# Kernel tuning notes

Hardware: AMD Instinct MI355X
Metric: run time of the kernel (lower is better)

The kernel has to match this reference:

```python
import jax, jax.numpy as jnp
import numpy as np

B, D, L = 4, 512, 4096
N1, N2 = 1167, 8921


def setup_inputs() -> dict:
    key = jax.random.key(0)
    k1, k2, k3, k4 = jax.random.split(key, 4)
    H = jax.random.normal(k1, (B, D, L), dtype=jnp.float32)
    Q1_w = jax.random.normal(k2, (N1, D), dtype=jnp.float32) * (1.0 / np.sqrt(D))
    Q2_w = jax.random.normal(k3, (N2, D), dtype=jnp.float32) * (1.0 / np.sqrt(D))
    Q12_w = jax.random.normal(k4, (N2, N1), dtype=jnp.float32) * (1.0 / np.sqrt(N1))
    return {"H": H, "Q1_w": Q1_w, "Q2_w": Q2_w, "Q12_w": Q12_w}


def reference(H, Q1_w, Q2_w, Q12_w):
    # H: [b, d, l]; Q1_w: [n1, d]; Q2_w: [n2, d]; Q12_w: [n2, n1]
    # Level-1 label attention
    E1 = jnp.einsum('nd,bdl->bnl', Q1_w, H)          # [b, n1, l]
    A1 = jax.nn.softmax(E1, axis=2)
    C1 = jnp.einsum('bnl,bdl->bnd', A1, H)           # [b, n1, d]
    # Project level-1 context to level-2 label space
    C1 = jnp.einsum('mn,bnd->bmd', Q12_w, C1)        # [b, n2, d]
    # Level-2 queries modulated by level-1 context (elementwise)
    Q2 = Q2_w[None, :, :] * C1                       # [b, n2, d]
    E2 = jnp.einsum('bmd,bdl->bml', Q2, H)           # [b, n2, l]
    A2 = jax.nn.softmax(E2, axis=2)
    C2 = jnp.einsum('bml,bdl->bmd', A2, H)           # [b, n2, d]
    return (C2, A2)
```

## Files before the change

kernel.cpp:

```cpp
#include <hip/hip_runtime.h>
#include <hip/hip_bf16.h>

typedef __bf16 bf16_t;
typedef __bf16 bf16x8 __attribute__((ext_vector_type(8)));
typedef __bf16 bf16x4 __attribute__((ext_vector_type(4)));
typedef float  f32x4  __attribute__((ext_vector_type(4)));

#define BM 128
#define BN 128
#define BK 64

__global__ __launch_bounds__(256) void cast_transpose_H(
    const float* __restrict__ H, bf16_t* __restrict__ Hb,
    bf16_t* __restrict__ HTb, int D, int L) {
  __shared__ bf16_t tile[32][33];
  int b = blockIdx.z;
  int l0 = blockIdx.x * 32, d0 = blockIdx.y * 32;
  const float* Hp = H + (size_t)b * D * L;
  bf16_t* Hbp = Hb + (size_t)b * D * L;
  bf16_t* HTp = HTb + (size_t)b * L * D;
  int tx = threadIdx.x, ty = threadIdx.y;
#pragma unroll
  for (int r = 0; r < 4; r++) {
    int d = d0 + ty + r * 8;
    float v = Hp[(size_t)d * L + l0 + tx];
    bf16_t bv = (bf16_t)v;
    tile[ty + r * 8][tx] = bv;
    Hbp[(size_t)d * L + l0 + tx] = bv;
  }
  __syncthreads();
#pragma unroll
  for (int r = 0; r < 4; r++) {
    int l = l0 + ty + r * 8;
    HTp[(size_t)l * D + d0 + tx] = tile[tx][ty + r * 8];
  }
}

__global__ void cast_w(const float* __restrict__ in, bf16_t* __restrict__ out, int n) {
  int i = blockIdx.x * 256 + threadIdx.x;
  if (i < n) out[i] = (bf16_t)in[i];
}

__global__ void cast_w_pad(const float* __restrict__ in, bf16_t* __restrict__ out,
                           int cols, int ldo) {
  int c = blockIdx.x * 256 + threadIdx.x;
  int r = blockIdx.y;
  if (c < ldo) {
    float v = (c < cols) ? in[(size_t)r * cols + c] : 0.0f;
    out[(size_t)r * ldo + c] = (bf16_t)v;
  }
}

__global__ void zero_pad(bf16_t* __restrict__ p, int n1, int ld, int rows) {
  int i = blockIdx.x * 256 + threadIdx.x;
  int padw = ld - n1;
  int r = i / padw, c = i - r * padw;
  if (r < rows) p[(size_t)r * ld + n1 + c] = (bf16_t)0.0f;
}

__device__ inline bf16x8 cvt8(float4 a, float4 b) {
  bf16x8 o;
  o[0] = (bf16_t)a.x; o[1] = (bf16_t)a.y; o[2] = (bf16_t)a.z; o[3] = (bf16_t)a.w;
  o[4] = (bf16_t)b.x; o[5] = (bf16_t)b.y; o[6] = (bf16_t)b.z; o[7] = (bf16_t)b.w;
  return o;
}

__device__ inline void gload_lds16(const bf16_t* g, bf16_t* l) {
  __builtin_amdgcn_global_load_lds(
      (const __attribute__((address_space(1))) void*)g,
      (__attribute__((address_space(3))) void*)l, 16, 0, 0);
}

__device__ inline void stage_half(const bf16_t* __restrict__ src, int ld,
                                  bf16_t* lds_half, int t, int wid) {
  int r = t >> 3;
  int gsl = (t & 7) ^ (r & 7);
  const bf16_t* g = src + (size_t)r * ld + gsl * 8;
  gload_lds16(g, lds_half + wid * 512);
  gload_lds16(g + (size_t)64 * ld, lds_half + 4096 + wid * 512);
}

template <int EPI>
__global__ __launch_bounds__(512) void gemm256_bt(
    const bf16_t* __restrict__ A, long sAb, const bf16_t* __restrict__ BT, long sBb,
    void* __restrict__ Cv, long sCb, const float* __restrict__ W,
    int M, int N, int K, int lda, int ldb, int ldc) {
  __shared__ __align__(16) bf16_t As[2][256][64];
  __shared__ __align__(16) bf16_t Bs[2][256][64];
  int b = blockIdx.z;
  A += (size_t)b * sAb;
  BT += (size_t)b * sBb;

  int nx = gridDim.x, ny = gridDim.y;
  int nwg = nx * ny;
  int bid = blockIdx.x + nx * blockIdx.y;
  int qq = nwg >> 3, rr = nwg & 7;
  int xcd = bid & 7, lin = bid >> 3;
  int swz = (xcd < rr ? xcd * (qq + 1) : rr * (qq + 1) + (xcd - rr) * qq) + lin;
  int m0 = (swz / ny) * 256;
  int n0 = (swz % ny) * 256;

  int t = threadIdx.x;
  int lane = t & 63, wid = t >> 6;
  int l15 = lane & 15, q = lane >> 4;
  int wm = (wid >> 2) * 128;
  int wn = (wid & 3) * 64;
  int NT = K >> 6;

  f32x4 acc[8][4];
#pragma unroll
  for (int i = 0; i < 8; i++)
#pragma unroll
    for (int j = 0; j < 4; j++)
#pragma unroll
      for (int e = 0; e < 4; e++) acc[i][j][e] = 0.0f;

  stage_half(BT + (size_t)(n0 + 0) * ldb, ldb, &Bs[0][0][0], t, wid);
  stage_half(BT + (size_t)(n0 + 128) * ldb, ldb, &Bs[0][128][0], t, wid);
  stage_half(A + (size_t)(m0 + 0) * lda, lda, &As[0][0][0], t, wid);
  stage_half(A + (size_t)(m0 + 128) * lda, lda, &As[0][128][0], t, wid);
  stage_half(BT + (size_t)(n0 + 0) * ldb + 64, ldb, &Bs[1][0][0], t, wid);
  stage_half(BT + (size_t)(n0 + 128) * ldb + 64, ldb, &Bs[1][128][0], t, wid);
  asm volatile("s_waitcnt vmcnt(4)" ::: "memory");
  __builtin_amdgcn_s_barrier();

  bf16x8 af[4][2];
  bf16x8 bF[2][2][2];

  for (int kt = 0; kt < NT; ++kt) {
    int buf = kt & 1;
    const bf16_t* An = A + (size_t)m0 * lda + (size_t)(kt + 1) * 64;
    const bf16_t* Bn2 = BT + (size_t)n0 * ldb + (size_t)(kt + 2) * 64;

    auto readA = [&](int mh) {
#pragma unroll
      for (int i = 0; i < 4; i++) {
        const char* rowp = (const char*)&As[buf][wm + mh * 64 + i * 16 + l15][0];
#pragma unroll
        for (int ks = 0; ks < 2; ks++)
          af[i][ks] = *(const bf16x8*)(rowp + ((((ks * 4 + q) ^ (l15 & 7))) << 4));
      }
    };
    auto readB = [&](int ch) {
#pragma unroll
      for (int j = 0; j < 2; j++) {
        const char* rowp = (const char*)&Bs[buf][wn + ch * 32 + j * 16 + l15][0];
#pragma unroll
        for (int ks = 0; ks < 2; ks++)
          bF[ch][j][ks] = *(const bf16x8*)(rowp + ((((ks * 4 + q) ^ (l15 & 7))) << 4));
      }
    };
    auto mmaq = [&](int mh, int ch) {
      __builtin_amdgcn_s_setprio(1);
#pragma unroll
      for (int i = 0; i < 4; i++)
#pragma unroll
        for (int j = 0; j < 2; j++)
#pragma unroll
          for (int ks = 0; ks < 2; ks++)
            acc[mh * 4 + i][ch * 2 + j] = __builtin_amdgcn_mfma_f32_16x16x32_bf16(
                af[i][ks], bF[ch][j][ks], acc[mh * 4 + i][ch * 2 + j], 0, 0, 0);
      __builtin_amdgcn_s_setprio(0);
    };

    readA(0);
    readB(0);
    if (kt + 1 < NT) stage_half(An, lda, &As[buf ^ 1][0][0], t, wid);
    __builtin_amdgcn_s_barrier();
    mmaq(0, 0);
    __builtin_amdgcn_s_barrier();
    readB(1);
    if (kt + 1 < NT) stage_half(An + (size_t)128 * lda, lda, &As[buf ^ 1][128][0], t, wid);
    __builtin_amdgcn_s_barrier();
    mmaq(0, 1);
    __builtin_amdgcn_s_barrier();
    readA(1);
    if (kt + 2 < NT) stage_half(Bn2, ldb, &Bs[buf][0][0], t, wid);
    __builtin_amdgcn_s_barrier();
    mmaq(1, 0);
    __builtin_amdgcn_s_barrier();
    if (kt + 2 < NT) {
      stage_half(Bn2 + (size_t)128 * ldb, ldb, &Bs[buf][128][0], t, wid);
      asm volatile("s_waitcnt vmcnt(4)" ::: "memory");
    } else if (kt + 1 < NT) {
      asm volatile("s_waitcnt vmcnt(0)" ::: "memory");
    }
    __builtin_amdgcn_s_barrier();
    mmaq(1, 1);
    __builtin_amdgcn_s_barrier();
  }

#pragma unroll
  for (int ig = 0; ig < 8; ig++) {
    int rbase = m0 + wm + ig * 16 + q * 4;
#pragma unroll
    for (int jg = 0; jg < 4; jg++) {
      int c = n0 + wn + jg * 16 + l15;
#pragma unroll
      for (int r4 = 0; r4 < 4; r4++) {
        int r = rbase + r4;
        if (r < M) {
          float val = acc[ig][jg][r4];
          if (EPI == 0) {
            ((float*)Cv + (size_t)b * sCb)[(size_t)r * ldc + c] = val;
          } else {
            float w = W[(size_t)r * N + c];
            ((bf16_t*)Cv + (size_t)b * sCb)[(size_t)r * ldc + c] = (bf16_t)(val * w);
          }
        }
      }
    }
  }
}

template <typename AT, int EPI>
__global__ __launch_bounds__(256) void gemm_bt(
    const AT* __restrict__ A, long sAb, const bf16_t* __restrict__ BT, long sBb,
    void* __restrict__ Cv, long sCb, const float* __restrict__ W,
    int M, int N, int K, int lda, int ldb, int ldc) {
  constexpr bool AF32 = (sizeof(AT) == 4);
  __shared__ __align__(16) bf16_t As[BM][BK];
  __shared__ __align__(16) bf16_t Bs[BN][BK];
  int b = blockIdx.z;
  A += (size_t)b * sAb;
  BT += (size_t)b * sBb;

  int nx = gridDim.x, ny = gridDim.y;
  int nwg = nx * ny;
  int bid = blockIdx.x + nx * blockIdx.y;
  int qq = nwg >> 3, rr = nwg & 7;
  int xcd = bid & 7, lin = bid >> 3;
  int swz = (xcd < rr ? xcd * (qq + 1) : rr * (qq + 1) + (xcd - rr) * qq) + lin;
  int m0 = (swz / ny) * BM;
  int n0 = (swz % ny) * BN;

  int t = threadIdx.x;
  int lane = t & 63, wid = t >> 6;
  int l15 = lane & 15, q = lane >> 4;
  int wm = (wid >> 1) * 64, wn = (wid & 1) * 64;

  int r0 = t >> 3;
  int sl = t & 7;
  int gsl = sl ^ (r0 & 7);
  bf16_t* lA = &As[0][0] + (size_t)wid * 512;
  bf16_t* lB = &Bs[0][0] + (size_t)wid * 512;

  f32x4 acc[4][4];
#pragma unroll
  for (int i = 0; i < 4; i++)
#pragma unroll
    for (int j = 0; j < 4; j++)
#pragma unroll
      for (int e = 0; e < 4; e++) acc[i][j][e] = 0.0f;

  for (int kb = 0; kb < K; kb += BK) {
    float4 va[4][2];
    if constexpr (AF32) {
#pragma unroll
      for (int i = 0; i < 4; i++) {
        int gm = m0 + i * 32 + r0;
        if (gm < M) {
          const float4* p = (const float4*)(A + (size_t)gm * lda + kb + gsl * 8);
          va[i][0] = p[0];
          va[i][1] = p[1];
        } else {
          va[i][0] = make_float4(0.f, 0.f, 0.f, 0.f);
          va[i][1] = make_float4(0.f, 0.f, 0.f, 0.f);
        }
      }
    }
    __syncthreads();
#pragma unroll
    for (int i = 0; i < 4; i++)
      gload_lds16(BT + (size_t)(n0 + i * 32 + r0) * ldb + kb + gsl * 8,
                  lB + i * 2048);
    if constexpr (AF32) {
#pragma unroll
      for (int i = 0; i < 4; i++)
        *(bf16x8*)(&As[0][0] + (size_t)(i * 256 + t) * 8) = cvt8(va[i][0], va[i][1]);
    } else {
#pragma unroll
      for (int i = 0; i < 4; i++)
        gload_lds16(A + (size_t)(m0 + i * 32 + r0) * lda + kb + gsl * 8,
                    lA + i * 2048);
    }
    __syncthreads();

#pragma unroll
    for (int ks = 0; ks < 2; ks++) {
      bf16x8 af[4], bfr[4];
#pragma unroll
      for (int i = 0; i < 4; i++) {
        int row = wm + i * 16 + l15;
        int off = (ks * 64 + q * 16) ^ ((l15 & 7) << 4);
        af[i] = *(const bf16x8*)((const char*)&As[row][0] + off);
      }
#pragma unroll
      for (int j = 0; j < 4; j++) {
        int row = wn + j * 16 + l15;
        int off = (ks * 64 + q * 16) ^ ((l15 & 7) << 4);
        bfr[j] = *(const bf16x8*)((const char*)&Bs[row][0] + off);
      }
#pragma unroll
      for (int i = 0; i < 4; i++)
#pragma unroll
        for (int j = 0; j < 4; j++)
          acc[i][j] = __builtin_amdgcn_mfma_f32_16x16x32_bf16(af[i], bfr[j],
                                                              acc[i][j], 0, 0, 0);
    }
  }

#pragma unroll
  for (int i = 0; i < 4; i++) {
    int rbase = m0 + wm + i * 16 + q * 4;
#pragma unroll
    for (int j = 0; j < 4; j++) {
      int c = n0 + wn + j * 16 + l15;
#pragma unroll
      for (int r4 = 0; r4 < 4; r4++) {
        int r = rbase + r4;
        if (r < M) {
          float val = acc[i][j][r4];
          if (EPI == 0) {
            float* Cp = (float*)Cv + (size_t)b * sCb;
            Cp[(size_t)r * ldc + c] = val;
          } else if (EPI == 1) {
            bf16_t* Cp = (bf16_t*)Cv + (size_t)b * sCb;
            Cp[(size_t)c * ldc + r] = (bf16_t)val;
          } else {
            float w = W[(size_t)r * N + c];
            bf16_t* Cp = (bf16_t*)Cv + (size_t)b * sCb;
            Cp[(size_t)r * ldc + c] = (bf16_t)(val * w);
          }
        }
      }
    }
  }
}

template <int MODE>
__global__ __launch_bounds__(256) void softmax_rows(
    const float* __restrict__ in, void* __restrict__ out,
    bf16_t* __restrict__ out2, int L) {
  int row = blockIdx.x;
  const float* ip = in + (size_t)row * L;
  int t = threadIdx.x;
  int lane = t & 63, wid = t >> 6;
  float4 v[4];
  float m = -3.4e38f;
#pragma unroll
  for (int c = 0; c < 4; c++) {
    v[c] = ((const float4*)ip)[c * 256 + t];
    m = fmaxf(m, fmaxf(fmaxf(v[c].x, v[c].y), fmaxf(v[c].z, v[c].w)));
  }
#pragma unroll
  for (int off = 1; off < 64; off <<= 1) m = fmaxf(m, __shfl_xor(m, off));
  __shared__ float redm[4];
  __shared__ float reds[4];
  if (lane == 0) redm[wid] = m;
  __syncthreads();
  m = fmaxf(fmaxf(redm[0], redm[1]), fmaxf(redm[2], redm[3]));
  float s = 0.0f;
#pragma unroll
  for (int c = 0; c < 4; c++) {
    v[c].x = __expf(v[c].x - m);
    v[c].y = __expf(v[c].y - m);
    v[c].z = __expf(v[c].z - m);
    v[c].w = __expf(v[c].w - m);
    s += (v[c].x + v[c].y) + (v[c].z + v[c].w);
  }
#pragma unroll
  for (int off = 1; off < 64; off <<= 1) s += __shfl_xor(s, off);
  if (lane == 0) reds[wid] = s;
  __syncthreads();
  s = (reds[0] + reds[1]) + (reds[2] + reds[3]);
  float inv = 1.0f / s;
  if (MODE == 1) {
    bf16_t* op = (bf16_t*)out + (size_t)row * L;
#pragma unroll
    for (int c = 0; c < 4; c++) {
      bf16x4 o;
      o[0] = (bf16_t)(v[c].x * inv);
      o[1] = (bf16_t)(v[c].y * inv);
      o[2] = (bf16_t)(v[c].z * inv);
      o[3] = (bf16_t)(v[c].w * inv);
      *(bf16x4*)(op + ((size_t)c * 256 + t) * 4) = o;
    }
  } else {
    float* op = (float*)out + (size_t)row * L;
#pragma unroll
    for (int c = 0; c < 4; c++) {
      float fx = v[c].x * inv, fy = v[c].y * inv, fz = v[c].z * inv, fw = v[c].w * inv;
      ((float4*)op)[c * 256 + t] = make_float4(fx, fy, fz, fw);
      if (MODE == 2) {
        bf16x4 o;
        o[0] = (bf16_t)fx; o[1] = (bf16_t)fy; o[2] = (bf16_t)fz; o[3] = (bf16_t)fw;
        *(bf16x4*)(out2 + (size_t)row * L + ((size_t)c * 256 + t) * 4) = o;
      }
    }
  }
}

extern "C" void kernel_launch(void* const* d_in, const int* in_sizes, int n_in,
                              void* d_out, int out_size, void* d_ws, size_t ws_size,
                              hipStream_t stream) {
  const int B = 4, D = 512, L = 4096, N1 = 1167, N2 = 8921;
  const int N1K = 1216;
  const int M1P = 1280;
  const int M2P = 8960;
  const float* H = (const float*)d_in[0];
  const float* Q1w = (const float*)d_in[1];
  const float* Q2w = (const float*)d_in[2];
  const float* Q12w = (const float*)d_in[3];
  float* C2 = (float*)d_out;
  float* A2 = C2 + (size_t)B * N2 * D;

  char* ws = (char*)d_ws;
  size_t off = 0;
  auto alloc = [&](size_t bytes) -> void* {
    void* p = ws + off;
    off = (off + bytes + 255) & ~(size_t)255;
    return p;
  };
  bf16_t* Hb   = (bf16_t*)alloc((size_t)B * D * L * 2);
  bf16_t* HTb  = (bf16_t*)alloc((size_t)B * L * D * 2);
  bf16_t* Q1b  = (bf16_t*)alloc((size_t)M1P * D * 2);
  bf16_t* Q12b = (bf16_t*)alloc((size_t)M2P * N1K * 2);
  float*  E1   = (float*)alloc((size_t)B * N1 * L * 4);
  bf16_t* A1b  = (bf16_t*)alloc(((size_t)B * N1 + 128) * L * 2);
  bf16_t* C1Tb = (bf16_t*)alloc((size_t)B * D * N1K * 2);
  bf16_t* Q2b  = (bf16_t*)alloc(((size_t)B * N2 + 64) * D * 2);
  size_t a2b_bytes = ((size_t)B * N2 + 128) * (size_t)L * 2;
  bool useA2b = (ws_size > 0) && (off + a2b_bytes <= ws_size);
  bf16_t* A2b = (bf16_t*)alloc(a2b_bytes);

  cast_transpose_H<<<dim3(L / 32, D / 32, B), dim3(32, 8), 0, stream>>>(H, Hb, HTb, D, L);
  cast_w<<<(N1 * D + 255) / 256, 256, 0, stream>>>(Q1w, Q1b, N1 * D);
  cast_w_pad<<<dim3((N1K + 255) / 256, N2), 256, 0, stream>>>(Q12w, Q12b, N1, N1K);
  zero_pad<<<(B * D * (N1K - N1) + 255) / 256, 256, 0, stream>>>(C1Tb, N1, N1K, B * D);
  gemm256_bt<0><<<dim3(M1P / 256, L / 256, B), 512, 0, stream>>>(
      Q1b, 0, HTb, (long)L * D, E1, (long)N1 * L, nullptr, N1, L, D, D, D, L);
  softmax_rows<1><<<B * N1, 256, 0, stream>>>(E1, A1b, nullptr, L);
  gemm_bt<bf16_t, 1><<<dim3(M1P / BM, D / BN, B), 256, 0, stream>>>(
      A1b, (long)N1 * L, Hb, (long)D * L, C1Tb, (long)D * N1K, nullptr, N1, D, L, L, L, N1K);
  gemm256_bt<2><<<dim3(M2P / 256, D / 256, B), 512, 0, stream>>>(
      Q12b, 0, C1Tb, (long)D * N1K, Q2b, (long)N2 * D, Q2w, N2, D, N1K, N1K, N1K, D);
  gemm256_bt<0><<<dim3(M2P / 256, L / 256, B), 512, 0, stream>>>(
      Q2b, (long)N2 * D, HTb, (long)L * D, A2, (long)N2 * L, nullptr, N2, L, D, D, D, L);
  if (useA2b) {
    softmax_rows<2><<<B * N2, 256, 0, stream>>>(A2, A2, A2b, L);
    gemm256_bt<0><<<dim3(M2P / 256, D / 256, B), 512, 0, stream>>>(
        A2b, (long)N2 * L, Hb, (long)D * L, C2, (long)N2 * D, nullptr, N2, D, L, L, L, D);
  } else {
    softmax_rows<0><<<B * N2, 256, 0, stream>>>(A2, A2, nullptr, L);
    gemm_bt<float, 0><<<dim3(M2P / BM, D / BN, B), 256, 0, stream>>>(
        A2, (long)N2 * L, Hb, (long)D * L, C2, (long)N2 * D, nullptr, N2, D, L, L, L, D);
  }
}
```

Measured before the change: 1.713 ms.

## Rework level-1 pipeline layout and move several GEMMs to 128-tile kernel

Pads N1 to 1280 across Q1, Q12 and A1 buffers and zero-fills the padded rows. The softmax writes into the padded per-batch layout, and the A1·H GEMM is recomputed as H·A1ᵀ so C1ᵀ is stored with coalesced row-major writes instead of the transposed scatter. The level-1 E1 GEMM, the Q12 projection and the final A2·H GEMM switch from the 256-tile 512-thread kernel to the 128-tile kernel, which raises block count for the smaller-N launches. The 256-tile kernel's barriers move to inline asm. The tradeoff is extra padded compute and less per-block reuse in the large final GEMM.

```diff
diff --git a/kernel.cpp b/kernel.cpp
--- a/kernel.cpp
+++ b/kernel.cpp
@@ -9,6 +9,8 @@
 #define BM 128
 #define BN 128
 #define BK 64
+
+#define SBAR() asm volatile("s_barrier" ::: "memory")
 
 __global__ __launch_bounds__(256) void cast_transpose_H(
     const float* __restrict__ H, bf16_t* __restrict__ Hb,
@@ -51,11 +53,14 @@
   }
 }
 
-__global__ void zero_pad(bf16_t* __restrict__ p, int n1, int ld, int rows) {
-  int i = blockIdx.x * 256 + threadIdx.x;
-  int padw = ld - n1;
-  int r = i / padw, c = i - r * padw;
-  if (r < rows) p[(size_t)r * ld + n1 + c] = (bf16_t)0.0f;
+__global__ void zero_rows(bf16_t* __restrict__ p, int r0, int nr, long sb, int L) {
+  long i = (long)blockIdx.x * 256 + threadIdx.x;
+  int b = blockIdx.y;
+  long tot = (long)nr * L / 8;
+  if (i < tot) {
+    bf16x8 z = {};
+    *(bf16x8*)(p + ((long)b * sb + r0) * L + i * 8) = z;
+  }
 }
 
 __device__ inline bf16x8 cvt8(float4 a, float4 b) {
@@ -122,7 +127,7 @@
   stage_half(BT + (size_t)(n0 + 0) * ldb + 64, ldb, &Bs[1][0][0], t, wid);
   stage_half(BT + (size_t)(n0 + 128) * ldb + 64, ldb, &Bs[1][128][0], t, wid);
   asm volatile("s_waitcnt vmcnt(4)" ::: "memory");
-  __builtin_amdgcn_s_barrier();
+  SBAR();
 
   bf16x8 af[4][2];
   bf16x8 bF[2][2][2];
@@ -166,28 +171,28 @@
     readA(0);
     readB(0);
     if (kt + 1 < NT) stage_half(An, lda, &As[buf ^ 1][0][0], t, wid);
-    __builtin_amdgcn_s_barrier();
+    SBAR();
     mmaq(0, 0);
-    __builtin_amdgcn_s_barrier();
+    SBAR();
     readB(1);
     if (kt + 1 < NT) stage_half(An + (size_t)128 * lda, lda, &As[buf ^ 1][128][0], t, wid);
-    __builtin_amdgcn_s_barrier();
+    SBAR();
     mmaq(0, 1);
-    __builtin_amdgcn_s_barrier();
+    SBAR();
     readA(1);
     if (kt + 2 < NT) stage_half(Bn2, ldb, &Bs[buf][0][0], t, wid);
-    __builtin_amdgcn_s_barrier();
+    SBAR();
     mmaq(1, 0);
-    __builtin_amdgcn_s_barrier();
+    SBAR();
     if (kt + 2 < NT) {
       stage_half(Bn2 + (size_t)128 * ldb, ldb, &Bs[buf][128][0], t, wid);
       asm volatile("s_waitcnt vmcnt(4)" ::: "memory");
     } else if (kt + 1 < NT) {
       asm volatile("s_waitcnt vmcnt(0)" ::: "memory");
     }
-    __builtin_amdgcn_s_barrier();
+    SBAR();
     mmaq(1, 1);
-    __builtin_amdgcn_s_barrier();
+    SBAR();
   }
 
 #pragma unroll
@@ -201,12 +206,7 @@
         int r = rbase + r4;
         if (r < M) {
           float val = acc[ig][jg][r4];
-          if (EPI == 0) {
-            ((float*)Cv + (size_t)b * sCb)[(size_t)r * ldc + c] = val;
-          } else {
-            float w = W[(size_t)r * N + c];
-            ((bf16_t*)Cv + (size_t)b * sCb)[(size_t)r * ldc + c] = (bf16_t)(val * w);
-          }
+          ((float*)Cv + (size_t)b * sCb)[(size_t)r * ldc + c] = val;
         }
       }
     }
@@ -324,13 +324,13 @@
           if (EPI == 0) {
             float* Cp = (float*)Cv + (size_t)b * sCb;
             Cp[(size_t)r * ldc + c] = val;
-          } else if (EPI == 1) {
-            bf16_t* Cp = (bf16_t*)Cv + (size_t)b * sCb;
-            Cp[(size_t)c * ldc + r] = (bf16_t)val;
-          } else {
+          } else if (EPI == 2) {
             float w = W[(size_t)r * N + c];
             bf16_t* Cp = (bf16_t*)Cv + (size_t)b * sCb;
             Cp[(size_t)r * ldc + c] = (bf16_t)(val * w);
+          } else {
+            bf16_t* Cp = (bf16_t*)Cv + (size_t)b * sCb;
+            Cp[(size_t)r * ldc + c] = (bf16_t)val;
           }
         }
       }
@@ -341,9 +341,10 @@
 template <int MODE>
 __global__ __launch_bounds__(256) void softmax_rows(
     const float* __restrict__ in, void* __restrict__ out,
-    bf16_t* __restrict__ out2, int L) {
-  int row = blockIdx.x;
-  const float* ip = in + (size_t)row * L;
+    bf16_t* __restrict__ out2, int L, int ostr) {
+  long row_in = (long)blockIdx.y * gridDim.x + blockIdx.x;
+  long row_out = (long)blockIdx.y * ostr + blockIdx.x;
+  const float* ip = in + row_in * L;
   int t = threadIdx.x;
   int lane = t & 63, wid = t >> 6;
   float4 v[4];
@@ -376,7 +377,7 @@
   s = (reds[0] + reds[1]) + (reds[2] + reds[3]);
   float inv = 1.0f / s;
   if (MODE == 1) {
-    bf16_t* op = (bf16_t*)out + (size_t)row * L;
+    bf16_t* op = (bf16_t*)out + row_out * L;
 #pragma unroll
     for (int c = 0; c < 4; c++) {
       bf16x4 o;
@@ -387,7 +388,7 @@
       *(bf16x4*)(op + ((size_t)c * 256 + t) * 4) = o;
     }
   } else {
-    float* op = (float*)out + (size_t)row * L;
+    float* op = (float*)out + row_out * L;
 #pragma unroll
     for (int c = 0; c < 4; c++) {
       float fx = v[c].x * inv, fy = v[c].y * inv, fz = v[c].z * inv, fw = v[c].w * inv;
@@ -395,7 +396,7 @@
       if (MODE == 2) {
         bf16x4 o;
         o[0] = (bf16_t)fx; o[1] = (bf16_t)fy; o[2] = (bf16_t)fz; o[3] = (bf16_t)fw;
-        *(bf16x4*)(out2 + (size_t)row * L + ((size_t)c * 256 + t) * 4) = o;
+        *(bf16x4*)(out2 + row_out * L + ((size_t)c * 256 + t) * 4) = o;
       }
     }
   }
@@ -405,8 +406,7 @@
                               void* d_out, int out_size, void* d_ws, size_t ws_size,
                               hipStream_t stream) {
   const int B = 4, D = 512, L = 4096, N1 = 1167, N2 = 8921;
-  const int N1K = 1216;
-  const int M1P = 1280;
+  const int N1P = 1280;
   const int M2P = 8960;
   const float* H = (const float*)d_in[0];
   const float* Q1w = (const float*)d_in[1];
@@ -424,35 +424,39 @@
   };
   bf16_t* Hb   = (bf16_t*)alloc((size_t)B * D * L * 2);
   bf16_t* HTb  = (bf16_t*)alloc((size_t)B * L * D * 2);
-  bf16_t* Q1b  = (bf16_t*)alloc((size_t)M1P * D * 2);
-  bf16_t* Q12b = (bf16_t*)alloc((size_t)M2P * N1K * 2);
+  bf16_t* Q1b  = (bf16_t*)alloc((size_t)N1P * D * 2);
+  bf16_t* Q12b = (bf16_t*)alloc((size_t)M2P * N1P * 2);
   float*  E1   = (float*)alloc((size_t)B * N1 * L * 4);
-  bf16_t* A1b  = (bf16_t*)alloc(((size_t)B * N1 + 128) * L * 2);
-  bf16_t* C1Tb = (bf16_t*)alloc((size_t)B * D * N1K * 2);
+  bf16_t* A1b  = (bf16_t*)alloc((size_t)B * N1P * L * 2);
+  bf16_t* C1Tb = (bf16_t*)alloc((size_t)B * D * N1P * 2);
   bf16_t* Q2b  = (bf16_t*)alloc(((size_t)B * N2 + 64) * D * 2);
   size_t a2b_bytes = ((size_t)B * N2 + 128) * (size_t)L * 2;
   bool useA2b = (ws_size > 0) && (off + a2b_bytes <= ws_size);
   bf16_t* A2b = (bf16_t*)alloc(a2b_bytes);
 
   cast_transpose_H<<<dim3(L / 32, D / 32, B), dim3(32, 8), 0, stream>>>(H, Hb, HTb, D, L);
-  cast_w<<<(N1 * D + 255) / 256, 256, 0, stream>>>(Q1w, Q1b, N1 * D);
-  cast_w_pad<<<dim3((N1K + 255) / 256, N2), 256, 0, stream>>>(Q12w, Q12b, N1, N1K);
-  zero_pad<<<(B * D * (N1K - N1) + 255) / 256, 256, 0, stream>>>(C1Tb, N1, N1K, B * D);
-  gemm256_bt<0><<<dim3(M1P / 256, L / 256, B), 512, 0, stream>>>(
+  cast_w_pad<<<dim3((D + 255) / 256, N1P), 256, 0, stream>>>(Q1w, Q1b, D, D);
+  zero_rows<<<dim3(((N1P - N1) * D / 8 + 255) / 256, 1), 256, 0, stream>>>(
+      Q1b, N1, N1P - N1, 0, D);
+  cast_w_pad<<<dim3((N1P + 255) / 256, N2), 256, 0, stream>>>(Q12w, Q12b, N1, N1P);
+  zero_rows<<<dim3(((N1P - N1) * L / 8 + 255) / 256, B), 256, 0, stream>>>(
+      A1b, N1, N1P - N1, (long)N1P, L);
+  gemm_bt<bf16_t, 0><<<dim3(N1P / BM, L / BN, B), 256, 0, stream>>>(
       Q1b, 0, HTb, (long)L * D, E1, (long)N1 * L, nullptr, N1, L, D, D, D, L);
-  softmax_rows<1><<<B * N1, 256, 0, stream>>>(E1, A1b, nullptr, L);
-  gemm_bt<bf16_t, 1><<<dim3(M1P / BM, D / BN, B), 256, 0, stream>>>(
-      A1b, (long)N1 * L, Hb, (long)D * L, C1Tb, (long)D * N1K, nullptr, N1, D, L, L, L, N1K);
-  gemm256_bt<2><<<dim3(M2P / 256, D / 256, B), 512, 0, stream>>>(
-      Q12b, 0, C1Tb, (long)D * N1K, Q2b, (long)N2 * D, Q2w, N2, D, N1K, N1K, N1K, D);
+  softmax_rows<1><<<dim3(N1, B), 256, 0, stream>>>(E1, A1b, nullptr, L, N1P);
+  gemm_bt<bf16_t, 3><<<dim3(D / BM, N1P / BN, B), 256, 0, stream>>>(
+      Hb, (long)D * L, A1b, (long)N1P * L, C1Tb, (long)D * N1P, nullptr,
+      D, N1P, L, L, L, N1P);
+  gemm_bt<bf16_t, 2><<<dim3(M2P / BM, D / BN, B), 256, 0, stream>>>(
+      Q12b, 0, C1Tb, (long)D * N1P, Q2b, (long)N2 * D, Q2w, N2, D, N1P, N1P, N1P, D);
   gemm256_bt<0><<<dim3(M2P / 256, L / 256, B), 512, 0, stream>>>(
       Q2b, (long)N2 * D, HTb, (long)L * D, A2, (long)N2 * L, nullptr, N2, L, D, D, D, L);
   if (useA2b) {
-    softmax_rows<2><<<B * N2, 256, 0, stream>>>(A2, A2, A2b, L);
-    gemm256_bt<0><<<dim3(M2P / 256, D / 256, B), 512, 0, stream>>>(
+    softmax_rows<2><<<dim3(B * N2, 1), 256, 0, stream>>>(A2, A2, A2b, L, 0);
+    gemm_bt<bf16_t, 0><<<dim3(M2P / BM, D / BN, B), 256, 0, stream>>>(
         A2b, (long)N2 * L, Hb, (long)D * L, C2, (long)N2 * D, nullptr, N2, D, L, L, L, D);
   } else {
-    softmax_rows<0><<<B * N2, 256, 0, stream>>>(A2, A2, nullptr, L);
+    softmax_rows<0><<<dim3(B * N2, 1), 256, 0, stream>>>(A2, A2, nullptr, L, 0);
     gemm_bt<float, 0><<<dim3(M2P / BM, D / BN, B), 256, 0, stream>>>(
         A2, (long)N2 * L, Hb, (long)D * L, C2, (long)N2 * D, nullptr, N2, D, L, L, L, D);
   }
```

New measurement: 1.649 ms. 3.8% less time.
